# Performance work log

Measured on AMD Instinct MI355X. Metric: run time of the kernel, lower is better.

## Reference

```python
import jax, jax.numpy as jnp
import numpy as np

B, N, C = 4, 1024, 23          # batch, nodes, scalar input channels (Rs_in=[(23,0)])
NB, H = 3, 100                 # cosine basis size, radial MLP hidden width
MAX_R = 3.0                    # CosineBasisModel max_radius
D1, D2, D3 = 30, 10, 1         # fc1/fc2/fc3 head dims


def setup_inputs() -> dict:
    key = jax.random.key(0)
    ks = jax.random.split(key, 12)
    features = jax.random.normal(ks[0], (B, N, C), jnp.float32)
    # random points inside a box comparable to max_radius so edges hit the basis support
    geometry = jax.random.uniform(ks[1], (B, N, 3), jnp.float32) * MAX_R
    # radial MLP (CosineBasisModel): NB -> H (relu) -> C weights (l=0 -> l=0 path, mul 23*1)
    W_rb1 = jax.random.normal(ks[2], (NB, H), jnp.float32) / np.sqrt(NB)
    b_rb1 = jnp.zeros((H,), jnp.float32)
    W_rb2 = jax.random.normal(ks[3], (H, C), jnp.float32) / np.sqrt(H)
    b_rb2 = jnp.zeros((C,), jnp.float32)
    # dense MLP head: Linear(N,30) -> Linear(30,10) -> Linear(10,1)
    W_fc1 = jax.random.normal(ks[4], (N, D1), jnp.float32) / np.sqrt(N)
    b_fc1 = jnp.zeros((D1,), jnp.float32)
    W_fc2 = jax.random.normal(ks[5], (D1, D2), jnp.float32) / np.sqrt(D1)
    b_fc2 = jnp.zeros((D2,), jnp.float32)
    W_fc3 = jax.random.normal(ks[6], (D2, D3), jnp.float32) / np.sqrt(D2)
    b_fc3 = jnp.zeros((D3,), jnp.float32)
    return {
        "features": features, "geometry": geometry,
        "W_rb1": W_rb1, "b_rb1": b_rb1, "W_rb2": W_rb2, "b_rb2": b_rb2,
        "W_fc1": W_fc1, "b_fc1": b_fc1, "W_fc2": W_fc2, "b_fc2": b_fc2,
        "W_fc3": W_fc3, "b_fc3": b_fc3,
    }


def _cosine_basis(r):
    """e3nn CosineBasisModel basis: cos^2 bumps centered on linspace(0,max_r,NB). r: [...]->[...,NB]."""
    radii = jnp.linspace(0.0, MAX_R, NB, dtype=r.dtype)
    step = radii[1] - radii[0]
    u = (r[..., None] - radii) / step
    half_pi = jnp.asarray(np.pi / 2, r.dtype)
    return jnp.where(jnp.abs(u) < 1.0, jnp.cos(half_pi * u) ** 2, jnp.zeros_like(u))


def reference(features, geometry, W_rb1, b_rb1, W_rb2, b_rb2,
              W_fc1, b_fc1, W_fc2, b_fc2, W_fc3, b_fc3):
    diff = geometry[:, :, None, :] - geometry[:, None, :, :]      # [B,N,N,3]
    r = jnp.sqrt(jnp.sum(diff * diff, axis=-1) + 1e-12)           # [B,N,N]
    basis = _cosine_basis(r)                                      # [B,N,N,NB]
    h = jax.nn.relu(basis @ W_rb1 + b_rb1)                        # [B,N,N,H]
    w = h @ W_rb2 + b_rb2                                         # [B,N,N,C] per-edge radial weights
    # scatter-sum weighted neighbor features -> scalar per node, 1/sqrt(N) kernel norm
    conv = jnp.einsum('zabc,zbc->za', w, features) / jnp.sqrt(jnp.asarray(N, w.dtype))  # [B,N]
    x = jax.nn.relu(conv @ W_fc1 + b_fc1)                         # [B,30]
    x = jax.nn.relu(x @ W_fc2 + b_fc2)                            # [B,10]
    x = x @ W_fc3 + b_fc3                                         # [B,1]
    return x
```

## Files before the change

### kernel.cpp

```cpp
#include <hip/hip_runtime.h>

#define Nn 1024
#define Cc 23
#define Hh 100
#define KN 64
#define DSTR 68
#define MUSCALE 14.0f
#define MUCLAMP 62.999f
#define NBC 512
#define NHB 30

#define UT_OFF     0
#define WF1T_OFF   1536
#define BIAS_OFF   32256
#define COLSUM_OFF 32260
#define CTR_OFF    32320
#define X1PRE_OFF  32384
#define PB_OFF     32512

__device__ __forceinline__ float rdlane(float v, int l) {
    return __int_as_float(__builtin_amdgcn_readlane(__float_as_int(v), l));
}

__global__ __launch_bounds__(256)
void prep_kernel(const float* __restrict__ f,
                 const float* __restrict__ W1,
                 const float* __restrict__ b1,
                 const float* __restrict__ W2,
                 const float* __restrict__ b2,
                 const float* __restrict__ Wf1,
                 float* __restrict__ ws) {
    int blk = blockIdx.x;
    int t = threadIdx.x;
    if (blk < 64) {
        __shared__ float w2s[Hh * Cc];
        __shared__ float hv_s[Hh];
        int k = blk;
        for (int j = t; j < Hh * Cc; j += 256) w2s[j] = W2[j];
        if (t < Hh) {
            float v = (float)k * (3.0f / 63.0f);
            const float HPI = 1.57079632679f;
            float c0 = cosf(HPI * v);
            float c1 = cosf(HPI * (v - 1.0f));
            float c2 = cosf(HPI * (v - 2.0f));
            float s0 = (v < 1.0f) ? c0 * c0 : 0.0f;
            float s1 = (fabsf(v - 1.0f) < 1.0f) ? c1 * c1 : 0.0f;
            float s2 = (v > 1.0f && v < 3.0f) ? c2 * c2 : 0.0f;
            float pre = fmaf(s0, W1[t],
                         fmaf(s1, W1[Hh + t],
                          fmaf(s2, W1[2 * Hh + t], b1[t])));
            hv_s[t] = fmaxf(pre, 0.f);
        }
        __syncthreads();
        if (t < Cc) {
            float a0 = 0.f, a1 = 0.f;
            #pragma unroll 4
            for (int h = 0; h < Hh; h += 2) {
                a0 = fmaf(hv_s[h],     w2s[h * Cc + t],       a0);
                a1 = fmaf(hv_s[h + 1], w2s[(h + 1) * Cc + t], a1);
            }
            ws[UT_OFF + t * KN + k] = a0 + a1;
        }
    } else if (blk < 94) {
        int d = blk - 64;
        #pragma unroll
        for (int j = 0; j < 4; ++j) {
            int k = j * 256 + t;
            ws[WF1T_OFF + d * Nn + k] = Wf1[k * 30 + d] * 0.03125f;
        }
    } else if (blk < 98) {
        __shared__ float red[256];
        int z = blk - 94;
        float s = 0.f;
        #pragma unroll
        for (int rr = 0; rr < 4; ++rr) {
            const float* fr = f + ((z << 10) + rr * 256 + t) * Cc;
            #pragma unroll
            for (int c = 0; c < Cc; ++c) s = fmaf(fr[c], b2[c], s);
        }
        red[t] = s; __syncthreads();
        for (int off = 128; off; off >>= 1) {
            if (t < off) red[t] += red[t + off];
            __syncthreads();
        }
        if (t == 0) ws[BIAS_OFF + z] = red[0];
    } else {
        __shared__ float cs_s[240];
        if (t < 240) {
            int d = t % 30, oct = t / 30;
            float c0 = 0.f, c1 = 0.f;
            #pragma unroll 4
            for (int j = 0; j < 128; j += 2) {
                c0 += Wf1[(oct * 128 + j) * 30 + d];
                c1 += Wf1[(oct * 128 + j + 1) * 30 + d];
            }
            cs_s[t] = c0 + c1;
        }
        __syncthreads();
        if (t < 30) {
            float cs = 0.f;
            #pragma unroll
            for (int o = 0; o < 8; ++o) cs += cs_s[o * 30 + t];
            ws[COLSUM_OFF + t] = cs;
        }
        if (t == 0) reinterpret_cast<unsigned*>(ws + CTR_OFF)[0] = 0u;
    }
}

__global__ __launch_bounds__(256, 2)
void conv_kernel(const float* __restrict__ f,
                 const float* __restrict__ geom,
                 const float* __restrict__ ut,
                 const float4* __restrict__ wf1t4,
                 float* __restrict__ pb) {
    __shared__ float lds_d[16 * DSTR];
    const int bid = blockIdx.x;
    const int t = threadIdx.x;
    const int lane = t & 63;
    const int q = __builtin_amdgcn_readfirstlane(t >> 6);
    const int z = bid >> 7;
    const int ah = (bid >> 6) & 1;
    const int s = bid & 63;
    const int b0 = s * 16;
    const int k = lane;

    float ur[Cc];
    #pragma unroll
    for (int c = 0; c < Cc; ++c) ur[c] = ut[c * KN + k];
    float fr[2];
    {
        int base = ((z << 10) + b0 + q * 4) * Cc;
        fr[0] = f[base + lane];
        int o2 = 64 + lane; if (o2 > 91) o2 = 91;
        fr[1] = f[base + o2];
    }
    float gr;
    {
        int off = lane < 48 ? lane : 47;
        gr = geom[((z << 10) + b0) * 3 + off];
    }
    int ag0 = ((z << 10) + (ah << 9) + t) * 3;
    float gax0 = geom[ag0], gay0 = geom[ag0 + 1], gaz0 = geom[ag0 + 2];
    int ag1 = ag0 + 768;
    float gax1 = geom[ag1], gay1 = geom[ag1 + 1], gaz1 = geom[ag1 + 2];

    #pragma unroll
    for (int r = 0; r < 4; ++r) {
        float a0 = 0.f, a1 = 0.f, a2 = 0.f, a3 = 0.f;
        #pragma unroll
        for (int c = 0; c < 20; c += 4) {
            a0 = fmaf(rdlane(fr[(r * Cc + c + 0) >> 6], (r * Cc + c + 0) & 63), ur[c + 0], a0);
            a1 = fmaf(rdlane(fr[(r * Cc + c + 1) >> 6], (r * Cc + c + 1) & 63), ur[c + 1], a1);
            a2 = fmaf(rdlane(fr[(r * Cc + c + 2) >> 6], (r * Cc + c + 2) & 63), ur[c + 2], a2);
            a3 = fmaf(rdlane(fr[(r * Cc + c + 3) >> 6], (r * Cc + c + 3) & 63), ur[c + 3], a3);
        }
        a0 = fmaf(rdlane(fr[(r * Cc + 20) >> 6], (r * Cc + 20) & 63), ur[20], a0);
        a1 = fmaf(rdlane(fr[(r * Cc + 21) >> 6], (r * Cc + 21) & 63), ur[21], a1);
        a2 = fmaf(rdlane(fr[(r * Cc + 22) >> 6], (r * Cc + 22) & 63), ur[22], a2);
        lds_d[(q * 4 + r) * DSTR + k] = (a0 + a1) + (a2 + a3);
    }
    __syncthreads();

    float acc0 = 0.f, acc1 = 0.f;
    #pragma unroll
    for (int bl = 0; bl < 16; ++bl) {
        float gbx = rdlane(gr, bl * 3 + 0);
        float gby = rdlane(gr, bl * 3 + 1);
        float gbz = rdlane(gr, bl * 3 + 2);
        const float* row = lds_d + bl * DSTR;
        {
            float dx = gax0 - gbx, dy = gay0 - gby, dz = gaz0 - gbz;
            float r = sqrtf(fmaf(dx, dx, fmaf(dy, dy, fmaf(dz, dz, 1e-12f))));
            float mu = fminf(r * MUSCALE, MUCLAMP);
            int m = (int)mu;
            float tt = mu - (float)m;
            float d0 = row[m], d1 = row[m + 1];
            acc0 += fmaf(tt, d1 - d0, d0);
        }
        {
            float dx = gax1 - gbx, dy = gay1 - gby, dz = gaz1 - gbz;
            float r = sqrtf(fmaf(dx, dx, fmaf(dy, dy, fmaf(dz, dz, 1e-12f))));
            float mu = fminf(r * MUSCALE, MUCLAMP);
            int m = (int)mu;
            float tt = mu - (float)m;
            float d0 = row[m], d1 = row[m + 1];
            acc1 += fmaf(tt, d1 - d0, d0);
        }
    }
    __syncthreads();

    lds_d[t] = acc0;
    lds_d[256 + t] = acc1;
    __syncthreads();
    {
        const float4* a4 = reinterpret_cast<const float4*>(lds_d);
        float4 av0 = a4[lane];
        float4 av1 = a4[64 + lane];
        #pragma unroll
        for (int i = 0; i < 8; ++i) {
            int d = q + 4 * i;
            if (d < 30) {
                float4 w0 = wf1t4[d * 256 + (ah << 7) + lane];
                float4 w1 = wf1t4[d * 256 + (ah << 7) + 64 + lane];
                float sum = av0.x * w0.x + av0.y * w0.y + av0.z * w0.z + av0.w * w0.w
                          + av1.x * w1.x + av1.y * w1.y + av1.z * w1.z + av1.w * w1.w;
                #pragma unroll
                for (int off = 32; off; off >>= 1) sum += __shfl_down(sum, off);
                if (lane == 0) pb[d * NBC + bid] = sum;
            }
        }
    }
}

__global__ __launch_bounds__(256)
void head_kernel(float* __restrict__ ws,
                 const float* __restrict__ bf1,
                 const float* __restrict__ Wf2, const float* __restrict__ bf2,
                 const float* __restrict__ Wf3, const float* __restrict__ bf3,
                 float* __restrict__ out) {
    __shared__ float x1s[120];
    __shared__ float x2s[40];
    __shared__ int lastflag;
    int d = blockIdx.x;
    int t = threadIdx.x;
    int z = t >> 6, lane = t & 63;
    {
        const float* p = ws + PB_OFF + d * NBC + (z << 7);
        float s = p[lane] + p[64 + lane];
        #pragma unroll
        for (int off = 32; off; off >>= 1) s += __shfl_down(s, off);
        if (lane == 0) ws[X1PRE_OFF + d * 4 + z] = s;
    }
    __syncthreads();
    if (t == 0) {
        unsigned* ctr = reinterpret_cast<unsigned*>(ws + CTR_OFF);
        unsigned r = __hip_atomic_fetch_add(ctr, 1u, __ATOMIC_ACQ_REL,
                                            __HIP_MEMORY_SCOPE_AGENT);
        lastflag = (r == NHB - 1) ? 1 : 0;
    }
    __syncthreads();
    if (!lastflag) return;

    if (t < 120) {
        int dd = t >> 2, zz = t & 3;
        float x1 = ws[X1PRE_OFF + t]
                 + ws[BIAS_OFF + zz] * 0.03125f * ws[COLSUM_OFF + dd]
                 + bf1[dd];
        x1s[zz * 30 + dd] = fmaxf(x1, 0.f);
    }
    __syncthreads();
    if (t < 40) {
        int zz = t / 10, dd = t % 10;
        float sm = bf2[dd];
        #pragma unroll
        for (int kk = 0; kk < 30; ++kk)
            sm = fmaf(x1s[zz * 30 + kk], Wf2[kk * 10 + dd], sm);
        x2s[t] = fmaxf(sm, 0.f);
    }
    __syncthreads();
    if (t < 4) {
        float sm = bf3[0];
        #pragma unroll
        for (int kk = 0; kk < 10; ++kk)
            sm = fmaf(x2s[t * 10 + kk], Wf3[kk], sm);
        out[t] = sm;
    }
}

extern "C" void kernel_launch(void* const* d_in, const int* in_sizes, int n_in,
                              void* d_out, int out_size, void* d_ws, size_t ws_size,
                              hipStream_t stream) {
    const float* f   = (const float*)d_in[0];
    const float* geo = (const float*)d_in[1];
    const float* W1  = (const float*)d_in[2];
    const float* b1  = (const float*)d_in[3];
    const float* W2  = (const float*)d_in[4];
    const float* b2  = (const float*)d_in[5];
    const float* Wf1 = (const float*)d_in[6];
    const float* bf1 = (const float*)d_in[7];
    const float* Wf2 = (const float*)d_in[8];
    const float* bf2 = (const float*)d_in[9];
    const float* Wf3 = (const float*)d_in[10];
    const float* bf3 = (const float*)d_in[11];
    float* ws  = (float*)d_ws;
    float* out = (float*)d_out;

    hipLaunchKernelGGL(prep_kernel, dim3(99), dim3(256), 0, stream,
                       f, W1, b1, W2, b2, Wf1, ws);
    hipLaunchKernelGGL(conv_kernel, dim3(NBC), dim3(256), 0, stream,
                       f, geo, ws + UT_OFF,
                       reinterpret_cast<const float4*>(ws + WF1T_OFF),
                       ws + PB_OFF);
    hipLaunchKernelGGL(head_kernel, dim3(NHB), dim3(256), 0, stream,
                       ws, bf1, Wf2, bf2, Wf3, bf3, out);
}
```

Before: 23.29 us.

## Split conv work across twice as many blocks and prefetch fc1 weights into registers

Doubles the conv grid: each block now covers a quarter of the target nodes, and each thread handles one target node instead of two. Occupancy bounds are raised to 4 blocks per SIMD. The fc1 weight slices are loaded into registers at kernel start, so their latency overlaps the basis contraction. The head kernel's partial-sum reduction is updated for the doubled partial buffer and now uses float4 loads. The intent is better latency hiding and CU coverage, at the cost of redundant per-block setup work and a larger partial buffer.

```diff
diff --git a/kernel.cpp b/kernel.cpp
--- a/kernel.cpp
+++ b/kernel.cpp
@@ -7,7 +7,7 @@
 #define DSTR 68
 #define MUSCALE 14.0f
 #define MUCLAMP 62.999f
-#define NBC 512
+#define NBC 1024
 #define NHB 30
 
 #define UT_OFF     0
@@ -107,7 +107,7 @@
     }
 }
 
-__global__ __launch_bounds__(256, 2)
+__global__ __launch_bounds__(256, 4)
 void conv_kernel(const float* __restrict__ f,
                  const float* __restrict__ geom,
                  const float* __restrict__ ut,
@@ -118,8 +118,8 @@
     const int t = threadIdx.x;
     const int lane = t & 63;
     const int q = __builtin_amdgcn_readfirstlane(t >> 6);
-    const int z = bid >> 7;
-    const int ah = (bid >> 6) & 1;
+    const int z = bid >> 8;
+    const int aq = (bid >> 6) & 3;
     const int s = bid & 63;
     const int b0 = s * 16;
     const int k = lane;
@@ -139,10 +139,15 @@
         int off = lane < 48 ? lane : 47;
         gr = geom[((z << 10) + b0) * 3 + off];
     }
-    int ag0 = ((z << 10) + (ah << 9) + t) * 3;
-    float gax0 = geom[ag0], gay0 = geom[ag0 + 1], gaz0 = geom[ag0 + 2];
-    int ag1 = ag0 + 768;
-    float gax1 = geom[ag1], gay1 = geom[ag1 + 1], gaz1 = geom[ag1 + 2];
+    int ag = ((z << 10) + (aq << 8) + t) * 3;
+    float gax = geom[ag], gay = geom[ag + 1], gaz = geom[ag + 2];
+    float4 wreg[8];
+    #pragma unroll
+    for (int i = 0; i < 8; ++i) {
+        int d = q + 4 * i;
+        wreg[i] = (d < 30) ? wf1t4[d * 256 + (aq << 6) + lane]
+                           : make_float4(0.f, 0.f, 0.f, 0.f);
+    }
 
     #pragma unroll
     for (int r = 0; r < 4; ++r) {
@@ -161,52 +166,36 @@
     }
     __syncthreads();
 
-    float acc0 = 0.f, acc1 = 0.f;
+    float acc = 0.f;
     #pragma unroll
     for (int bl = 0; bl < 16; ++bl) {
-        float gbx = rdlane(gr, bl * 3 + 0);
-        float gby = rdlane(gr, bl * 3 + 1);
-        float gbz = rdlane(gr, bl * 3 + 2);
-        const float* row = lds_d + bl * DSTR;
-        {
-            float dx = gax0 - gbx, dy = gay0 - gby, dz = gaz0 - gbz;
-            float r = sqrtf(fmaf(dx, dx, fmaf(dy, dy, fmaf(dz, dz, 1e-12f))));
-            float mu = fminf(r * MUSCALE, MUCLAMP);
-            int m = (int)mu;
-            float tt = mu - (float)m;
-            float d0 = row[m], d1 = row[m + 1];
-            acc0 += fmaf(tt, d1 - d0, d0);
-        }
-        {
-            float dx = gax1 - gbx, dy = gay1 - gby, dz = gaz1 - gbz;
-            float r = sqrtf(fmaf(dx, dx, fmaf(dy, dy, fmaf(dz, dz, 1e-12f))));
-            float mu = fminf(r * MUSCALE, MUCLAMP);
-            int m = (int)mu;
-            float tt = mu - (float)m;
-            float d0 = row[m], d1 = row[m + 1];
-            acc1 += fmaf(tt, d1 - d0, d0);
-        }
-    }
-    __syncthreads();
-
-    lds_d[t] = acc0;
-    lds_d[256 + t] = acc1;
+        float dx = gax - rdlane(gr, bl * 3 + 0);
+        float dy = gay - rdlane(gr, bl * 3 + 1);
+        float dz = gaz - rdlane(gr, bl * 3 + 2);
+        float r = sqrtf(fmaf(dx, dx, fmaf(dy, dy, fmaf(dz, dz, 1e-12f))));
+        float mu = fminf(r * MUSCALE, MUCLAMP);
+        int m = (int)mu;
+        float tt = mu - (float)m;
+        const float* row = lds_d + bl * DSTR + m;
+        float d0 = row[0], d1 = row[1];
+        acc += fmaf(tt, d1 - d0, d0);
+    }
+    __syncthreads();
+
+    lds_d[t] = acc;
     __syncthreads();
     {
         const float4* a4 = reinterpret_cast<const float4*>(lds_d);
-        float4 av0 = a4[lane];
-        float4 av1 = a4[64 + lane];
+        float4 av = a4[lane];
         #pragma unroll
         for (int i = 0; i < 8; ++i) {
             int d = q + 4 * i;
             if (d < 30) {
-                float4 w0 = wf1t4[d * 256 + (ah << 7) + lane];
-                float4 w1 = wf1t4[d * 256 + (ah << 7) + 64 + lane];
-                float sum = av0.x * w0.x + av0.y * w0.y + av0.z * w0.z + av0.w * w0.w
-                          + av1.x * w1.x + av1.y * w1.y + av1.z * w1.z + av1.w * w1.w;
+                float4 w = wreg[i];
+                float sum = av.x * w.x + av.y * w.y + av.z * w.z + av.w * w.w;
                 #pragma unroll
                 for (int off = 32; off; off >>= 1) sum += __shfl_down(sum, off);
-                if (lane == 0) pb[d * NBC + bid] = sum;
+                if (lane == 0) pb[d * NBC + (z << 8) + (aq << 6) + s] = sum;
             }
         }
     }
@@ -225,8 +214,9 @@
     int t = threadIdx.x;
     int z = t >> 6, lane = t & 63;
     {
-        const float* p = ws + PB_OFF + d * NBC + (z << 7);
-        float s = p[lane] + p[64 + lane];
+        const float4* p4 = reinterpret_cast<const float4*>(ws + PB_OFF + d * NBC);
+        float4 v = p4[t];
+        float s = (v.x + v.y) + (v.z + v.w);
         #pragma unroll
         for (int off = 32; off; off >>= 1) s += __shfl_down(s, off);
         if (lane == 0) ws[X1PRE_OFF + d * 4 + z] = s;
```

New measurement: 23.90 us. 2.6% more time.
